# Performance work log

Hardware: AMD Instinct MI355X
Metric: run time of the kernel (lower is better)

The kernel has to match this reference:

```python
import jax, jax.numpy as jnp
import numpy as np

N = 16384      # tokens (batch*seq)
D = 2048       # input_size / d_model
E = 64         # num_experts
K = 2          # top_k
EPS = 1e-12    # F.normalize eps


def setup_inputs() -> dict:
    key = jax.random.key(0)
    k1, k2 = jax.random.split(key)
    x = jax.random.normal(k1, (N, D), dtype=jnp.float32)
    # nn.Linear(input_size, num_experts, bias=False) weight has shape [E, D]
    W = jax.random.normal(k2, (E, D), dtype=jnp.float32) / np.sqrt(D)
    return {"x": x, "W": W}


def reference(x, W):
    # router logits: [N, E], computed (and kept) in float32 as in .float()
    logits = jnp.matmul(x, W.T).astype(jnp.float32)

    top_k_logits, top_k_indices = jax.lax.top_k(logits, K)      # [N, K]
    top_k_gates = jax.nn.softmax(top_k_logits, axis=1).astype(x.dtype)

    # ---- training-mode aux loss ----
    probs = jax.nn.softmax(logits, axis=1)                      # [N, E]
    rows = jnp.arange(logits.shape[0])[:, None]                 # [N, 1]
    gates = jnp.zeros_like(probs).astype(top_k_gates.dtype)
    gates = gates.at[rows, top_k_indices].set(top_k_gates)      # dense [N, E]

    count = logits.shape[0]
    p_sum = probs.sum(axis=0)                                   # [E]
    freq = (gates > 0).astype(jnp.float32).sum(axis=0)          # [E]
    lse = jax.nn.logsumexp(logits, axis=-1)                     # [N]
    lsesq = jnp.sum(lse ** 2)

    p_norm = p_sum / jnp.maximum(jnp.sum(jnp.abs(p_sum)), EPS)   # L1 normalize
    f_norm = freq / jnp.maximum(jnp.sum(jnp.abs(freq)), EPS)
    switchloss = E * jnp.sum(p_norm * f_norm)
    z_loss = lsesq / count
    loss = switchloss + 0.1 * z_loss

    return top_k_indices, top_k_gates, loss
```

## Files before the change

### kernel.cpp

```cpp
#include <hip/hip_runtime.h>
#include <hip/hip_bf16.h>
#include <math.h>

#define N_TOK 16384
#define D_DIM 2048
#define E_EXP 64
#define SPLIT 4
#define KPER  (D_DIM / SPLIT)
#define NCH   (KPER / 32)
#define NTILE (N_TOK / 64)

typedef __attribute__((ext_vector_type(8))) short bf16x8;
typedef __attribute__((ext_vector_type(4))) float f32x4;
typedef __attribute__((ext_vector_type(4))) unsigned int u32x4;

#define PACK2(HI, LO) __builtin_amdgcn_perm((HI), (LO), 0x07060302u)

__global__ void pack_w(const float* __restrict__ W,
                       unsigned short* __restrict__ Wp) {
  const int T = blockIdx.x * 256 + threadIdx.x;
  const int e = T & 63, g = (T >> 6) & 3, c = T >> 8;
  const float* src = W + (size_t)e * D_DIM + c * 32 + g * 8;
  float4 v0 = *(const float4*)src;
  float4 v1 = *(const float4*)(src + 4);
  float vv[8] = {v0.x, v0.y, v0.z, v0.w, v1.x, v1.y, v1.z, v1.w};
  unsigned hu[8], mu[8], lu[8];
#pragma unroll
  for (int j = 0; j < 8; ++j) {
    unsigned u = __float_as_uint(vv[j]);
    unsigned a = u & 0xffff0000u;
    float r = vv[j] - __uint_as_float(a);
    unsigned b = __float_as_uint(r) & 0xffff0000u;
    float r2 = r - __uint_as_float(b);
    unsigned d = __float_as_uint(r2) & 0xffff0000u;
    hu[j] = a; mu[j] = b; lu[j] = d;
  }
  unsigned ph[4], pm[4], pl[4];
#pragma unroll
  for (int q = 0; q < 4; ++q) {
    ph[q] = PACK2(hu[2 * q + 1], hu[2 * q]);
    pm[q] = PACK2(mu[2 * q + 1], mu[2 * q]);
    pl[q] = PACK2(lu[2 * q + 1], lu[2 * q]);
  }
  const size_t base = (size_t)c * 6144 + g * 1536 + e * 8;
  *(u32x4*)(Wp + base)        = *(u32x4*)ph;
  *(u32x4*)(Wp + base + 512)  = *(u32x4*)pm;
  *(u32x4*)(Wp + base + 1024) = *(u32x4*)pl;
}

__global__ __launch_bounds__(256)
void router_gemm(const float* __restrict__ x,
                 const unsigned short* __restrict__ Wp,
                 float* __restrict__ part) {
  __shared__ __align__(16) unsigned short s_x[2 * 3 * 64 * 32];
  const int tid  = threadIdx.x;
  const int lane = tid & 63;
  const int w    = tid >> 6;
  const int th   = w >> 1;
  const int eh   = w & 1;
  const int tile  = blockIdx.x & (NTILE - 1);
  const int split = blockIdx.x >> 8;
  const int T0 = tile * 64;
  const int k0 = split * KPER;

  const int crow = tid >> 2;
  const int ckg  = tid & 3;
  const float* xg = x + (size_t)(T0 + crow) * D_DIM + k0 + ckg * 8;
  const int wbase = crow * 32 + ((ckg ^ ((crow >> 1) & 3)) << 3);

  const int arow  = th * 32 + (lane & 15);
  const int abase = arow * 32 + ((((lane >> 4) ^ ((arow >> 1) & 3))) << 3);
  const int bl = (lane >> 4) * 1536 + (eh * 32 + (lane & 15)) * 8;

  f32x4 acc[2][2];
#pragma unroll
  for (int i = 0; i < 2; ++i)
#pragma unroll
    for (int j = 0; j < 2; ++j) acc[i][j] = (f32x4)0.f;

#define CVT_WRITE(BUF, V0, V1)                                              \
  do {                                                                      \
    float vv[8] = {V0.x, V0.y, V0.z, V0.w, V1.x, V1.y, V1.z, V1.w};         \
    unsigned hu[8], mu[8], lu[8];                                           \
    _Pragma("unroll") for (int j = 0; j < 8; ++j) {                         \
      unsigned u = __float_as_uint(vv[j]);                                  \
      unsigned a = u & 0xffff0000u;                                         \
      float r = vv[j] - __uint_as_float(a);                                 \
      unsigned b = __float_as_uint(r) & 0xffff0000u;                        \
      float r2 = r - __uint_as_float(b);                                    \
      unsigned d = __float_as_uint(r2) & 0xffff0000u;                       \
      hu[j] = a; mu[j] = b; lu[j] = d;                                      \
    }                                                                       \
    unsigned ph[4], pm[4], pl[4];                                           \
    _Pragma("unroll") for (int q = 0; q < 4; ++q) {                         \
      ph[q] = PACK2(hu[2 * q + 1], hu[2 * q]);                              \
      pm[q] = PACK2(mu[2 * q + 1], mu[2 * q]);                              \
      pl[q] = PACK2(lu[2 * q + 1], lu[2 * q]);                              \
    }                                                                       \
    *(u32x4*)&s_x[(BUF) * 6144 + 0 * 2048 + wbase] = *(u32x4*)ph;           \
    *(u32x4*)&s_x[(BUF) * 6144 + 1 * 2048 + wbase] = *(u32x4*)pm;           \
    *(u32x4*)&s_x[(BUF) * 6144 + 2 * 2048 + wbase] = *(u32x4*)pl;           \
  } while (0)

  float4 rx0 = *(const float4*)xg;
  float4 rx1 = *(const float4*)(xg + 4);
  CVT_WRITE(0, rx0, rx1);
  rx0 = *(const float4*)(xg + 32);
  rx1 = *(const float4*)(xg + 36);
  __syncthreads();

  const unsigned short* bp = Wp + (size_t)(split * NCH) * 6144 + bl;

#pragma unroll 1
  for (int c = 0; c < NCH; ++c) {
    const int buf = c & 1;
    if (c + 1 < NCH) CVT_WRITE(buf ^ 1, rx0, rx1);
    if (c + 2 < NCH) {
      rx0 = *(const float4*)(xg + (c + 2) * 32);
      rx1 = *(const float4*)(xg + (c + 2) * 32 + 4);
    }
    bf16x8 B0h = *(const bf16x8*)(bp);
    bf16x8 B0m = *(const bf16x8*)(bp + 512);
    bf16x8 B0l = *(const bf16x8*)(bp + 1024);
    bf16x8 B1h = *(const bf16x8*)(bp + 128);
    bf16x8 B1m = *(const bf16x8*)(bp + 128 + 512);
    bf16x8 B1l = *(const bf16x8*)(bp + 128 + 1024);
    const unsigned short* ab = &s_x[buf * 6144 + abase];
    bf16x8 A0h = *(const bf16x8*)(ab);
    bf16x8 A0m = *(const bf16x8*)(ab + 2048);
    bf16x8 A0l = *(const bf16x8*)(ab + 4096);
    bf16x8 A1h = *(const bf16x8*)(ab + 512);
    bf16x8 A1m = *(const bf16x8*)(ab + 512 + 2048);
    bf16x8 A1l = *(const bf16x8*)(ab + 512 + 4096);

#define MM(AH, AM, AL, BH, BM, BL, ACC)                                       \
    ACC = __builtin_amdgcn_mfma_f32_16x16x32_bf16(AH, BH, ACC, 0, 0, 0);      \
    ACC = __builtin_amdgcn_mfma_f32_16x16x32_bf16(AH, BM, ACC, 0, 0, 0);      \
    ACC = __builtin_amdgcn_mfma_f32_16x16x32_bf16(AM, BH, ACC, 0, 0, 0);      \
    ACC = __builtin_amdgcn_mfma_f32_16x16x32_bf16(AH, BL, ACC, 0, 0, 0);      \
    ACC = __builtin_amdgcn_mfma_f32_16x16x32_bf16(AM, BM, ACC, 0, 0, 0);      \
    ACC = __builtin_amdgcn_mfma_f32_16x16x32_bf16(AL, BH, ACC, 0, 0, 0)

    MM(A0h, A0m, A0l, B0h, B0m, B0l, acc[0][0]);
    MM(A0h, A0m, A0l, B1h, B1m, B1l, acc[0][1]);
    MM(A1h, A1m, A1l, B0h, B0m, B0l, acc[1][0]);
    MM(A1h, A1m, A1l, B1h, B1m, B1l, acc[1][1]);
#undef MM
    bp += 6144;
    __syncthreads();
  }
#undef CVT_WRITE

  const int r0 = (lane >> 4) * 4;
  const int cc = lane & 15;
#pragma unroll
  for (int mt = 0; mt < 2; ++mt)
#pragma unroll
    for (int rr = 0; rr < 4; ++rr) {
      const int t = T0 + th * 32 + mt * 16 + r0 + rr;
      float* p = part + ((size_t)split * N_TOK + t) * 64 + eh * 32 + cc;
      p[0]  = acc[mt][0][rr];
      p[16] = acc[mt][1][rr];
    }
}

__global__ __launch_bounds__(64)
void epilogue(const float* __restrict__ part, int nsplit,
              float* __restrict__ out,
              double* __restrict__ blk_ps,
              double* __restrict__ blk_z,
              unsigned* __restrict__ freq) {
  const int lane = threadIdx.x;
  const int t    = blockIdx.x * 64 + lane;

  float l[64];
  {
    const float* p0 = part + (size_t)t * 64;
#pragma unroll
    for (int q = 0; q < 16; ++q) {
      float4 a = *(const float4*)(p0 + q * 4);
      l[q * 4 + 0] = a.x; l[q * 4 + 1] = a.y;
      l[q * 4 + 2] = a.z; l[q * 4 + 3] = a.w;
    }
  }
  for (int s = 1; s < nsplit; ++s) {
    const float* ps = part + ((size_t)s * N_TOK + t) * 64;
#pragma unroll
    for (int q = 0; q < 16; ++q) {
      float4 a = *(const float4*)(ps + q * 4);
      l[q * 4 + 0] += a.x; l[q * 4 + 1] += a.y;
      l[q * 4 + 2] += a.z; l[q * 4 + 3] += a.w;
    }
  }

  float m = l[0];
#pragma unroll
  for (int e = 1; e < 64; ++e) m = fmaxf(m, l[e]);

  float sum = 0.f;
#pragma unroll
  for (int e = 0; e < 64; ++e) sum += __expf(l[e] - m);
  const float lse = m + __logf(sum);
  const float inv = 1.0f / sum;

  float v0 = l[0], v1 = -3.402823466e38f;
  int i0 = 0, i1 = 0;
#pragma unroll
  for (int e = 1; e < 64; ++e) {
    float le = l[e];
    bool g0 = le > v0;
    bool g1 = le > v1;
    float nv1 = g0 ? v0 : (g1 ? le : v1);
    int   ni1 = g0 ? i0 : (g1 ? e  : i1);
    float nv0 = g0 ? le : v0;
    int   ni0 = g0 ? e  : i0;
    v0 = nv0; i0 = ni0; v1 = nv1; i1 = ni1;
  }

  float d  = __expf(v1 - v0);
  float g0 = 1.0f / (1.0f + d);
  float g1 = d * g0;

  out[t * 2 + 0] = (float)i0;
  out[t * 2 + 1] = (float)i1;
  out[2 * N_TOK + t * 2 + 0] = g0;
  out[2 * N_TOK + t * 2 + 1] = g1;

  __shared__ unsigned hist[64];
  hist[lane] = 0u;
  __syncthreads();
  atomicAdd(&hist[i0], 1u);
  atomicAdd(&hist[i1], 1u);
  __syncthreads();
  if (hist[lane]) atomicAdd(&freq[lane], hist[lane]);

  float myps = 0.f;
#pragma unroll
  for (int e = 0; e < 64; ++e) {
    float v = __expf(l[e] - m) * inv;
    v += __shfl_xor(v, 32, 64);
    v += __shfl_xor(v, 16, 64);
    v += __shfl_xor(v, 8, 64);
    v += __shfl_xor(v, 4, 64);
    v += __shfl_xor(v, 2, 64);
    v += __shfl_xor(v, 1, 64);
    myps = (lane == e) ? v : myps;
  }
  blk_ps[(size_t)blockIdx.x * 64 + lane] = (double)myps;

  float z = lse * lse;
  z += __shfl_xor(z, 32, 64);
  z += __shfl_xor(z, 16, 64);
  z += __shfl_xor(z, 8, 64);
  z += __shfl_xor(z, 4, 64);
  z += __shfl_xor(z, 2, 64);
  z += __shfl_xor(z, 1, 64);
  if (lane == 0) blk_z[blockIdx.x] = (double)z;
}

__global__ void finalize(const double* __restrict__ blk_ps,
                         const double* __restrict__ blk_z,
                         const unsigned* __restrict__ freq,
                         float* __restrict__ out_loss) {
  const int lane = threadIdx.x;
  double p = 0.0;
  for (int b = 0; b < 256; ++b) p += blk_ps[(size_t)b * 64 + lane];
  double zt = 0.0;
#pragma unroll
  for (int b = 0; b < 4; ++b) zt += blk_z[lane * 4 + b];
#pragma unroll
  for (int off = 32; off >= 1; off >>= 1) zt += __shfl_xor(zt, off, 64);

  double f = (double)freq[lane];
  double pa = fabs(p);
  double fa = fabs(f);
#pragma unroll
  for (int off = 32; off >= 1; off >>= 1) {
    pa += __shfl_xor(pa, off, 64);
    fa += __shfl_xor(fa, off, 64);
  }
  pa = pa > 1e-12 ? pa : 1e-12;
  fa = fa > 1e-12 ? fa : 1e-12;

  double s = (p / pa) * (f / fa);
#pragma unroll
  for (int off = 32; off >= 1; off >>= 1) s += __shfl_xor(s, off, 64);

  if (lane == 0) {
    double switchloss = 64.0 * s;
    double z_loss = zt / (double)N_TOK;
    out_loss[0] = (float)(switchloss + 0.1 * z_loss);
  }
}

extern "C" void kernel_launch(void* const* d_in, const int* in_sizes, int n_in,
                              void* d_out, int out_size, void* d_ws, size_t ws_size,
                              hipStream_t stream) {
  const float* x = (const float*)d_in[0];
  const float* W = (const float*)d_in[1];
  float* out = (float*)d_out;

  const size_t partB = (size_t)N_TOK * 64 * 4;
  float* part = (float*)d_ws;
  size_t off = (size_t)SPLIT * partB;
  double* blk_ps = (double*)((char*)d_ws + off);
  double* blk_z  = blk_ps + 256 * 64;
  unsigned* freq = (unsigned*)(blk_z + 256);
  size_t woff = (off + 256 * 64 * 8 + 256 * 8 + 64 * 4 + 255) & ~(size_t)255;
  unsigned short* Wp = (unsigned short*)((char*)d_ws + woff);

  hipMemsetAsync(freq, 0, 64 * sizeof(unsigned), stream);

  pack_w<<<64, 256, 0, stream>>>(W, Wp);
  router_gemm<<<NTILE * SPLIT, 256, 0, stream>>>(x, Wp, part);
  epilogue<<<N_TOK / 64, 64, 0, stream>>>(part, SPLIT, out, blk_ps, blk_z, freq);
  finalize<<<1, 64, 0, stream>>>(blk_ps, blk_z, freq, out + 4 * N_TOK);
}
```

Baseline: 62.77 us.

## Fuse router GEMM with softmax/top-k epilogue, drop split-K partials

Replaces the split-K GEMM plus separate epilogue with one kernel per 64-token tile that runs the full K reduction with 512 threads (8 waves, each owning 16 tokens by 32 experts) and does softmax, top-2, histogram and per-expert prob sums from shared memory. This removes the global round trip of four partial logit buffers and one launch. The shared x tile gets a padded row stride instead of an XOR swizzle. The trade-off is fewer blocks (256) each walking all 64 K-chunks serially, and an epilogue handled by only one or two waves while the rest idle.

```diff
diff --git a/kernel.cpp b/kernel.cpp
--- a/kernel.cpp
+++ b/kernel.cpp
@@ -5,16 +5,19 @@
 #define N_TOK 16384
 #define D_DIM 2048
 #define E_EXP 64
-#define SPLIT 4
-#define KPER  (D_DIM / SPLIT)
-#define NCH   (KPER / 32)
-#define NTILE (N_TOK / 64)
+#define NCH   64
+#define NBLK  (N_TOK / 64)
 
 typedef __attribute__((ext_vector_type(8))) short bf16x8;
 typedef __attribute__((ext_vector_type(4))) float f32x4;
 typedef __attribute__((ext_vector_type(4))) unsigned int u32x4;
+typedef __attribute__((ext_vector_type(2))) unsigned int u32x2;
 
 #define PACK2(HI, LO) __builtin_amdgcn_perm((HI), (LO), 0x07060302u)
+
+#define XROW 40
+#define PLANE (64 * XROW)
+#define BUFSZ (3 * PLANE)
 
 __global__ void pack_w(const float* __restrict__ W,
                        unsigned short* __restrict__ Wp) {
@@ -48,41 +51,44 @@
   *(u32x4*)(Wp + base + 1024) = *(u32x4*)pl;
 }
 
-__global__ __launch_bounds__(256)
-void router_gemm(const float* __restrict__ x,
-                 const unsigned short* __restrict__ Wp,
-                 float* __restrict__ part) {
-  __shared__ __align__(16) unsigned short s_x[2 * 3 * 64 * 32];
+__global__ __launch_bounds__(512)
+void fused_router(const float* __restrict__ x,
+                  const unsigned short* __restrict__ Wp,
+                  float* __restrict__ out,
+                  double* __restrict__ blk_ps,
+                  double* __restrict__ blk_z,
+                  unsigned* __restrict__ freq) {
+  __shared__ __align__(16) unsigned short s_x[2 * BUFSZ];
+  __shared__ float s_l[64 * 66];
+  __shared__ unsigned hist[64];
   const int tid  = threadIdx.x;
   const int lane = tid & 63;
   const int w    = tid >> 6;
   const int th   = w >> 1;
   const int eh   = w & 1;
-  const int tile  = blockIdx.x & (NTILE - 1);
-  const int split = blockIdx.x >> 8;
-  const int T0 = tile * 64;
-  const int k0 = split * KPER;
-
-  const int crow = tid >> 2;
-  const int ckg  = tid & 3;
-  const float* xg = x + (size_t)(T0 + crow) * D_DIM + k0 + ckg * 8;
-  const int wbase = crow * 32 + ((ckg ^ ((crow >> 1) & 3)) << 3);
-
-  const int arow  = th * 32 + (lane & 15);
-  const int abase = arow * 32 + ((((lane >> 4) ^ ((arow >> 1) & 3))) << 3);
-  const int bl = (lane >> 4) * 1536 + (eh * 32 + (lane & 15)) * 8;
-
-  f32x4 acc[2][2];
-#pragma unroll
-  for (int i = 0; i < 2; ++i)
-#pragma unroll
-    for (int j = 0; j < 2; ++j) acc[i][j] = (f32x4)0.f;
-
-#define CVT_WRITE(BUF, V0, V1)                                              \
+  const int T0   = blockIdx.x * 64;
+
+  if (tid < 64) hist[tid] = 0u;
+
+  const int crow = tid >> 3;
+  const int cs   = tid & 7;
+  const float* xg = x + (size_t)(T0 + crow) * D_DIM + cs * 4;
+  const int wbase = crow * XROW + cs * 4;
+
+  const int arow  = th * 16 + (lane & 15);
+  const int abase = arow * XROW + (lane >> 4) * 8;
+  const unsigned short* bp =
+      Wp + (lane >> 4) * 1536 + (eh * 32 + (lane & 15)) * 8;
+
+  f32x4 acc[2];
+  acc[0] = (f32x4)0.f;
+  acc[1] = (f32x4)0.f;
+
+#define CVT4(BUF, V)                                                        \
   do {                                                                      \
-    float vv[8] = {V0.x, V0.y, V0.z, V0.w, V1.x, V1.y, V1.z, V1.w};         \
-    unsigned hu[8], mu[8], lu[8];                                           \
-    _Pragma("unroll") for (int j = 0; j < 8; ++j) {                         \
+    float vv[4] = {(V).x, (V).y, (V).z, (V).w};                             \
+    unsigned hu[4], mu[4], lu[4];                                           \
+    _Pragma("unroll") for (int j = 0; j < 4; ++j) {                         \
       unsigned u = __float_as_uint(vv[j]);                                  \
       unsigned a = u & 0xffff0000u;                                         \
       float r = vv[j] - __uint_as_float(a);                                 \
@@ -91,171 +97,124 @@
       unsigned d = __float_as_uint(r2) & 0xffff0000u;                       \
       hu[j] = a; mu[j] = b; lu[j] = d;                                      \
     }                                                                       \
-    unsigned ph[4], pm[4], pl[4];                                           \
-    _Pragma("unroll") for (int q = 0; q < 4; ++q) {                         \
-      ph[q] = PACK2(hu[2 * q + 1], hu[2 * q]);                              \
-      pm[q] = PACK2(mu[2 * q + 1], mu[2 * q]);                              \
-      pl[q] = PACK2(lu[2 * q + 1], lu[2 * q]);                              \
-    }                                                                       \
-    *(u32x4*)&s_x[(BUF) * 6144 + 0 * 2048 + wbase] = *(u32x4*)ph;           \
-    *(u32x4*)&s_x[(BUF) * 6144 + 1 * 2048 + wbase] = *(u32x4*)pm;           \
-    *(u32x4*)&s_x[(BUF) * 6144 + 2 * 2048 + wbase] = *(u32x4*)pl;           \
+    u32x2 vh = {PACK2(hu[1], hu[0]), PACK2(hu[3], hu[2])};                  \
+    u32x2 vm = {PACK2(mu[1], mu[0]), PACK2(mu[3], mu[2])};                  \
+    u32x2 vl = {PACK2(lu[1], lu[0]), PACK2(lu[3], lu[2])};                  \
+    *(u32x2*)&s_x[(BUF) * BUFSZ + wbase]             = vh;                  \
+    *(u32x2*)&s_x[(BUF) * BUFSZ + PLANE + wbase]     = vm;                  \
+    *(u32x2*)&s_x[(BUF) * BUFSZ + 2 * PLANE + wbase] = vl;                  \
   } while (0)
 
-  float4 rx0 = *(const float4*)xg;
-  float4 rx1 = *(const float4*)(xg + 4);
-  CVT_WRITE(0, rx0, rx1);
-  rx0 = *(const float4*)(xg + 32);
-  rx1 = *(const float4*)(xg + 36);
+  float4 rx = *(const float4*)xg;
+  CVT4(0, rx);
+  rx = *(const float4*)(xg + 32);
   __syncthreads();
-
-  const unsigned short* bp = Wp + (size_t)(split * NCH) * 6144 + bl;
 
 #pragma unroll 1
   for (int c = 0; c < NCH; ++c) {
     const int buf = c & 1;
-    if (c + 1 < NCH) CVT_WRITE(buf ^ 1, rx0, rx1);
-    if (c + 2 < NCH) {
-      rx0 = *(const float4*)(xg + (c + 2) * 32);
-      rx1 = *(const float4*)(xg + (c + 2) * 32 + 4);
-    }
+    if (c + 1 < NCH) CVT4(buf ^ 1, rx);
+    if (c + 2 < NCH) rx = *(const float4*)(xg + (c + 2) * 32);
     bf16x8 B0h = *(const bf16x8*)(bp);
     bf16x8 B0m = *(const bf16x8*)(bp + 512);
     bf16x8 B0l = *(const bf16x8*)(bp + 1024);
     bf16x8 B1h = *(const bf16x8*)(bp + 128);
     bf16x8 B1m = *(const bf16x8*)(bp + 128 + 512);
     bf16x8 B1l = *(const bf16x8*)(bp + 128 + 1024);
-    const unsigned short* ab = &s_x[buf * 6144 + abase];
-    bf16x8 A0h = *(const bf16x8*)(ab);
-    bf16x8 A0m = *(const bf16x8*)(ab + 2048);
-    bf16x8 A0l = *(const bf16x8*)(ab + 4096);
-    bf16x8 A1h = *(const bf16x8*)(ab + 512);
-    bf16x8 A1m = *(const bf16x8*)(ab + 512 + 2048);
-    bf16x8 A1l = *(const bf16x8*)(ab + 512 + 4096);
-
-#define MM(AH, AM, AL, BH, BM, BL, ACC)                                       \
-    ACC = __builtin_amdgcn_mfma_f32_16x16x32_bf16(AH, BH, ACC, 0, 0, 0);      \
-    ACC = __builtin_amdgcn_mfma_f32_16x16x32_bf16(AH, BM, ACC, 0, 0, 0);      \
-    ACC = __builtin_amdgcn_mfma_f32_16x16x32_bf16(AM, BH, ACC, 0, 0, 0);      \
-    ACC = __builtin_amdgcn_mfma_f32_16x16x32_bf16(AH, BL, ACC, 0, 0, 0);      \
-    ACC = __builtin_amdgcn_mfma_f32_16x16x32_bf16(AM, BM, ACC, 0, 0, 0);      \
-    ACC = __builtin_amdgcn_mfma_f32_16x16x32_bf16(AL, BH, ACC, 0, 0, 0)
-
-    MM(A0h, A0m, A0l, B0h, B0m, B0l, acc[0][0]);
-    MM(A0h, A0m, A0l, B1h, B1m, B1l, acc[0][1]);
-    MM(A1h, A1m, A1l, B0h, B0m, B0l, acc[1][0]);
-    MM(A1h, A1m, A1l, B1h, B1m, B1l, acc[1][1]);
+    const unsigned short* ab = &s_x[buf * BUFSZ + abase];
+    bf16x8 Ah = *(const bf16x8*)(ab);
+    bf16x8 Am = *(const bf16x8*)(ab + PLANE);
+    bf16x8 Al = *(const bf16x8*)(ab + 2 * PLANE);
+
+#define MM(BH, BM, BL, ACC)                                                   \
+    ACC = __builtin_amdgcn_mfma_f32_16x16x32_bf16(Ah, BH, ACC, 0, 0, 0);      \
+    ACC = __builtin_amdgcn_mfma_f32_16x16x32_bf16(Ah, BM, ACC, 0, 0, 0);      \
+    ACC = __builtin_amdgcn_mfma_f32_16x16x32_bf16(Am, BH, ACC, 0, 0, 0);      \
+    ACC = __builtin_amdgcn_mfma_f32_16x16x32_bf16(Ah, BL, ACC, 0, 0, 0);      \
+    ACC = __builtin_amdgcn_mfma_f32_16x16x32_bf16(Am, BM, ACC, 0, 0, 0);      \
+    ACC = __builtin_amdgcn_mfma_f32_16x16x32_bf16(Al, BH, ACC, 0, 0, 0)
+
+    MM(B0h, B0m, B0l, acc[0]);
+    MM(B1h, B1m, B1l, acc[1]);
 #undef MM
     bp += 6144;
     __syncthreads();
   }
-#undef CVT_WRITE
-
-  const int r0 = (lane >> 4) * 4;
-  const int cc = lane & 15;
-#pragma unroll
-  for (int mt = 0; mt < 2; ++mt)
+#undef CVT4
+
+  {
+    const int tok = th * 16 + (lane >> 4) * 4;
+    const int ex  = eh * 32 + (lane & 15);
 #pragma unroll
     for (int rr = 0; rr < 4; ++rr) {
-      const int t = T0 + th * 32 + mt * 16 + r0 + rr;
-      float* p = part + ((size_t)split * N_TOK + t) * 64 + eh * 32 + cc;
-      p[0]  = acc[mt][0][rr];
-      p[16] = acc[mt][1][rr];
+      s_l[(tok + rr) * 66 + ex]      = acc[0][rr];
+      s_l[(tok + rr) * 66 + ex + 16] = acc[1][rr];
     }
-}
-
-__global__ __launch_bounds__(64)
-void epilogue(const float* __restrict__ part, int nsplit,
-              float* __restrict__ out,
-              double* __restrict__ blk_ps,
-              double* __restrict__ blk_z,
-              unsigned* __restrict__ freq) {
-  const int lane = threadIdx.x;
-  const int t    = blockIdx.x * 64 + lane;
-
-  float l[64];
-  {
-    const float* p0 = part + (size_t)t * 64;
-#pragma unroll
-    for (int q = 0; q < 16; ++q) {
-      float4 a = *(const float4*)(p0 + q * 4);
-      l[q * 4 + 0] = a.x; l[q * 4 + 1] = a.y;
-      l[q * 4 + 2] = a.z; l[q * 4 + 3] = a.w;
+  }
+  __syncthreads();
+
+  if (tid < 64) {
+    const int t = tid;
+    float m = -3.402823466e38f;
+#pragma unroll
+    for (int e = 0; e < 64; ++e) m = fmaxf(m, s_l[t * 66 + e]);
+    float sum = 0.f;
+#pragma unroll
+    for (int e = 0; e < 64; ++e) sum += __expf(s_l[t * 66 + e] - m);
+    const float lse = m + __logf(sum);
+    const float inv = 1.0f / sum;
+    s_l[t * 66 + 64] = m;
+    s_l[t * 66 + 65] = inv;
+
+    float v0 = s_l[t * 66 + 0], v1 = -3.402823466e38f;
+    int i0 = 0, i1 = 0;
+#pragma unroll
+    for (int e = 1; e < 64; ++e) {
+      float le = s_l[t * 66 + e];
+      bool g0 = le > v0;
+      bool g1 = le > v1;
+      float nv1 = g0 ? v0 : (g1 ? le : v1);
+      int   ni1 = g0 ? i0 : (g1 ? e  : i1);
+      v0 = g0 ? le : v0;
+      i0 = g0 ? e  : i0;
+      v1 = nv1; i1 = ni1;
     }
-  }
-  for (int s = 1; s < nsplit; ++s) {
-    const float* ps = part + ((size_t)s * N_TOK + t) * 64;
-#pragma unroll
-    for (int q = 0; q < 16; ++q) {
-      float4 a = *(const float4*)(ps + q * 4);
-      l[q * 4 + 0] += a.x; l[q * 4 + 1] += a.y;
-      l[q * 4 + 2] += a.z; l[q * 4 + 3] += a.w;
+    float dd = __expf(v1 - v0);
+    float g0 = 1.0f / (1.0f + dd);
+    float g1 = dd * g0;
+
+    const int tg = T0 + t;
+    out[tg * 2 + 0] = (float)i0;
+    out[tg * 2 + 1] = (float)i1;
+    out[2 * N_TOK + tg * 2 + 0] = g0;
+    out[2 * N_TOK + tg * 2 + 1] = g1;
+
+    atomicAdd(&hist[i0], 1u);
+    atomicAdd(&hist[i1], 1u);
+
+    float z = lse * lse;
+    z += __shfl_xor(z, 32, 64);
+    z += __shfl_xor(z, 16, 64);
+    z += __shfl_xor(z, 8, 64);
+    z += __shfl_xor(z, 4, 64);
+    z += __shfl_xor(z, 2, 64);
+    z += __shfl_xor(z, 1, 64);
+    if (lane == 0) blk_z[blockIdx.x] = (double)z;
+  }
+  __syncthreads();
+
+  if (w == 1) {
+    const int e = lane;
+    float cs2 = 0.f;
+#pragma unroll 8
+    for (int t = 0; t < 64; ++t) {
+      float m   = s_l[t * 66 + 64];
+      float inv = s_l[t * 66 + 65];
+      cs2 += __expf(s_l[t * 66 + e] - m) * inv;
     }
-  }
-
-  float m = l[0];
-#pragma unroll
-  for (int e = 1; e < 64; ++e) m = fmaxf(m, l[e]);
-
-  float sum = 0.f;
-#pragma unroll
-  for (int e = 0; e < 64; ++e) sum += __expf(l[e] - m);
-  const float lse = m + __logf(sum);
-  const float inv = 1.0f / sum;
-
-  float v0 = l[0], v1 = -3.402823466e38f;
-  int i0 = 0, i1 = 0;
-#pragma unroll
-  for (int e = 1; e < 64; ++e) {
-    float le = l[e];
-    bool g0 = le > v0;
-    bool g1 = le > v1;
-    float nv1 = g0 ? v0 : (g1 ? le : v1);
-    int   ni1 = g0 ? i0 : (g1 ? e  : i1);
-    float nv0 = g0 ? le : v0;
-    int   ni0 = g0 ? e  : i0;
-    v0 = nv0; i0 = ni0; v1 = nv1; i1 = ni1;
-  }
-
-  float d  = __expf(v1 - v0);
-  float g0 = 1.0f / (1.0f + d);
-  float g1 = d * g0;
-
-  out[t * 2 + 0] = (float)i0;
-  out[t * 2 + 1] = (float)i1;
-  out[2 * N_TOK + t * 2 + 0] = g0;
-  out[2 * N_TOK + t * 2 + 1] = g1;
-
-  __shared__ unsigned hist[64];
-  hist[lane] = 0u;
-  __syncthreads();
-  atomicAdd(&hist[i0], 1u);
-  atomicAdd(&hist[i1], 1u);
-  __syncthreads();
-  if (hist[lane]) atomicAdd(&freq[lane], hist[lane]);
-
-  float myps = 0.f;
-#pragma unroll
-  for (int e = 0; e < 64; ++e) {
-    float v = __expf(l[e] - m) * inv;
-    v += __shfl_xor(v, 32, 64);
-    v += __shfl_xor(v, 16, 64);
-    v += __shfl_xor(v, 8, 64);
-    v += __shfl_xor(v, 4, 64);
-    v += __shfl_xor(v, 2, 64);
-    v += __shfl_xor(v, 1, 64);
-    myps = (lane == e) ? v : myps;
-  }
-  blk_ps[(size_t)blockIdx.x * 64 + lane] = (double)myps;
-
-  float z = lse * lse;
-  z += __shfl_xor(z, 32, 64);
-  z += __shfl_xor(z, 16, 64);
-  z += __shfl_xor(z, 8, 64);
-  z += __shfl_xor(z, 4, 64);
-  z += __shfl_xor(z, 2, 64);
-  z += __shfl_xor(z, 1, 64);
-  if (lane == 0) blk_z[blockIdx.x] = (double)z;
+    blk_ps[(size_t)blockIdx.x * 64 + e] = (double)cs2;
+  }
+  if (tid < 64 && hist[tid]) atomicAdd(&freq[tid], hist[tid]);
 }
 
 __global__ void finalize(const double* __restrict__ blk_ps,
@@ -300,19 +259,15 @@
   const float* W = (const float*)d_in[1];
   float* out = (float*)d_out;
 
-  const size_t partB = (size_t)N_TOK * 64 * 4;
-  float* part = (float*)d_ws;
-  size_t off = (size_t)SPLIT * partB;
-  double* blk_ps = (double*)((char*)d_ws + off);
+  double* blk_ps = (double*)d_ws;
   double* blk_z  = blk_ps + 256 * 64;
   unsigned* freq = (unsigned*)(blk_z + 256);
-  size_t woff = (off + 256 * 64 * 8 + 256 * 8 + 64 * 4 + 255) & ~(size_t)255;
+  size_t woff = (256 * 64 * 8 + 256 * 8 + 64 * 4 + 255) & ~(size_t)255;
   unsigned short* Wp = (unsigned short*)((char*)d_ws + woff);
 
   hipMemsetAsync(freq, 0, 64 * sizeof(unsigned), stream);
 
   pack_w<<<64, 256, 0, stream>>>(W, Wp);
-  router_gemm<<<NTILE * SPLIT, 256, 0, stream>>>(x, Wp, part);
-  epilogue<<<N_TOK / 64, 64, 0, stream>>>(part, SPLIT, out, blk_ps, blk_z, freq);
+  fused_router<<<NBLK, 512, 0, stream>>>(x, Wp, out, blk_ps, blk_z, freq);
   finalize<<<1, 64, 0, stream>>>(blk_ps, blk_z, freq, out + 4 * N_TOK);
 }
```

Measured after the change: 83.13 us. +32.4%, slower.
